# Kernel tuning notes

Hardware: AMD Instinct MI355X
Metric: run time of the kernel (lower is better)

The kernel has to match this reference:

```python
import jax, jax.numpy as jnp
import numpy as np

N_ENTITY = 30000
N_MOVIE = 6000
D = 384            # entity_hidden_size = hidden_size // 2
H = 768            # hidden_size
HT = 768           # token_hidden_size
N_LAYER = 12
N_BLOCK = 2
N_HEAD = 12
HEAD_DIM = H // N_HEAD
NUM_REL = 12
NUM_BASES = 8
E_KG = 200000
E_C = 200000
E_S = 80000
B = 16
LE = 48
LT = 256


def setup_inputs() -> dict:
    key = jax.random.key(0)
    ks = iter(jax.random.split(key, 48))
    nk = lambda: next(ks)
    rn = lambda shape, s=0.02: jax.random.normal(nk(), shape, dtype=jnp.float32) * s
    ri = lambda shape, m: jax.random.randint(nk(), shape, 0, m)
    return {
        'node_embeds': rn((N_ENTITY, D), 0.05),
        'rgcn_bases': rn((NUM_BASES, D, D)),
        'rgcn_comp': rn((NUM_REL, NUM_BASES), 0.3),
        'rgcn_root': rn((D, D)),
        'rgcn_bias': rn((D,), 0.01),
        'ep1_w1': rn((D, D // 2)), 'ep1_b1': rn((D // 2,), 0.01),
        'ep1_w2': rn((D // 2, D)), 'ep1_b2': rn((D,), 0.01),
        'ep2_w': rn((D, H)), 'ep2_b': rn((H,), 0.01),
        'tp1_w1': rn((HT, HT // 2)), 'tp1_b1': rn((HT // 2,), 0.01),
        'tp1_w2': rn((HT // 2, HT)), 'tp1_b2': rn((HT,), 0.01),
        'tp2_w': rn((HT, H)), 'tp2_b': rn((H,), 0.01),
        'ca_w': rn((H, H)),
        'pp1_w1': rn((H, H // 2)), 'pp1_b1': rn((H // 2,), 0.01),
        'pp1_w2': rn((H // 2, H)), 'pp1_b2': rn((H,), 0.01),
        'pp2_w': rn((H, N_LAYER * N_BLOCK * H)), 'pp2_b': rn((N_LAYER * N_BLOCK * H,), 0.01),
        'token_embeds': jax.random.normal(nk(), (B, LT, HT), dtype=jnp.float32),
        'edge_index': ri((2, E_KG), N_ENTITY),
        'edge_type': ri((E_KG,), NUM_REL),
        'edge_index_c': ri((2, E_C), N_ENTITY),
        'edge_index_t_s': ri((2, E_S), N_MOVIE),
        'edge_index_i_s': ri((2, E_S), N_MOVIE),
        'movie_to_entity': ri((N_MOVIE,), N_ENTITY),
        'entity_ids': ri((B, LE), N_ENTITY),
    }


def _mlp(x, w1, b1, w2, b2):
    return jax.nn.relu(x @ w1 + b1) @ w2 + b2


def _gcn(x, edge_index):
    # CustomGCNConv: add self loops, symmetric deg^{-1/2} norm, scatter-add
    n = x.shape[0]
    loop = jnp.arange(n)
    src = jnp.concatenate([edge_index[0], loop])
    dst = jnp.concatenate([edge_index[1], loop])
    deg = jax.ops.segment_sum(jnp.ones_like(dst, dtype=x.dtype), dst, num_segments=n)
    dis = deg ** -0.5  # deg >= 1 due to self loops
    norm = dis[src] * dis[dst]
    return jax.ops.segment_sum(norm[:, None] * x[src], dst, num_segments=n)


def _rgcn(x, edge_index, edge_type, bases, comp, root, bias):
    # PyG RGCNConv with basis decomposition, mean aggregation per relation
    n = x.shape[0]
    src, dst = edge_index[0], edge_index[1]
    W = jnp.einsum('rb,bio->rio', comp, bases)  # [R, D, D]
    out = x @ root + bias
    for r in range(NUM_REL):
        mask = (edge_type == r).astype(x.dtype)
        cnt = jax.ops.segment_sum(mask, dst, num_segments=n)
        norm = mask / jnp.maximum(cnt[dst], 1.0)
        h = x @ W[r]
        out = out + jax.ops.segment_sum(norm[:, None] * h[src], dst, num_segments=n)
    return out


def reference(node_embeds, rgcn_bases, rgcn_comp, rgcn_root, rgcn_bias,
              ep1_w1, ep1_b1, ep1_w2, ep1_b2, ep2_w, ep2_b,
              tp1_w1, tp1_b1, tp1_w2, tp1_b2, tp2_w, tp2_b,
              ca_w, pp1_w1, pp1_b1, pp1_w2, pp1_b2, pp2_w, pp2_b,
              token_embeds, edge_index, edge_type, edge_index_c,
              edge_index_t_s, edge_index_i_s, movie_to_entity, entity_ids):
    # ---- get_entity_embeds ----
    ent0 = _rgcn(node_embeds, edge_index, edge_type, rgcn_bases, rgcn_comp, rgcn_root, rgcn_bias) + node_embeds
    nf = ent0[movie_to_entity]  # sorted_indices == idx_to_id_tensor (keys are range(n_movie))
    ts1 = _gcn(nf, edge_index_t_s)
    ts2 = _gcn(ts1, edge_index_t_s)  # ts3 computed in original but unused -> skipped
    mt = (ts1 + ts2) * 0.5
    is1 = _gcn(nf, edge_index_i_s)
    is2 = _gcn(is1, edge_index_i_s)
    mi = (is1 + is2) * 0.5
    mm = (mt + mi) * 0.5
    c1 = _gcn(ent0, edge_index_c)
    c2 = _gcn(c1, edge_index_c)
    c3 = _gcn(c2, edge_index_c)
    ent = (c1 + c2 + c3 + ent0) * 0.25
    ent = ent.at[movie_to_entity].add(mm)  # index_add_
    ent = _mlp(ent, ep1_w1, ep1_b1, ep1_w2, ep1_b2) + ent
    ent = ent @ ep2_w + ep2_b  # [N_ENTITY, H]
    # ---- forward ----
    eemb = ent[entity_ids]  # [B, LE, H]
    tok = _mlp(token_embeds, tp1_w1, tp1_b1, tp1_w2, tp1_b2) + token_embeds
    tok = tok @ tp2_w + tp2_b  # [B, LT, H]
    attn = jnp.einsum('bth,beh->bte', tok @ ca_w, eemb) / H
    w = jax.nn.softmax(attn, axis=2)  # output_entity=False branch
    prompt = jnp.einsum('bte,beh->bth', w, eemb) + tok
    prompt = _mlp(prompt, pp1_w1, pp1_b1, pp1_w2, pp1_b2) + prompt
    prompt = prompt @ pp2_w + pp2_b  # [B, LT, N_LAYER*N_BLOCK*H]
    prompt = prompt.reshape(B, LT, N_LAYER, N_BLOCK, N_HEAD, HEAD_DIM)
    return prompt.transpose(2, 3, 0, 4, 1, 5)  # [n_layer, n_block, B, n_head, LT, head_dim]
```

## Files before the change

kernel.cpp:

```cpp
#include <hip/hip_runtime.h>
#include <hip/hip_bf16.h>
#include <cstdint>
#include <cstddef>


namespace {

constexpr int NE   = 30000;
constexpr int NM   = 6000;
constexpr int Dm   = 384;
constexpr int Hm   = 768;
constexpr int EKG  = 200000;
constexpr int EC   = 200000;
constexpr int ES   = 80000;
constexpr int Bc   = 16;
constexpr int LE   = 48;
constexpr int NTOK = 4096;
constexpr int NO   = 18432;

constexpr size_t NBf = (size_t)NE * Dm;
constexpr size_t MBF = (size_t)NM * Dm;

constexpr size_t P_XB    = 0;
constexpr size_t P_WCT   = 5760000;
constexpr size_t P_CNT   = 6644736;
constexpr size_t P_ENT0  = 7004736;
constexpr size_t P_HH    = 18524736;
constexpr size_t P_DIS   = 53084736;
constexpr size_t P_E0B   = 0;
constexpr size_t P_C1B   = 2880000;
constexpr size_t P_C2B   = 5760000;
constexpr size_t P_NFB   = 8640000;
constexpr size_t P_T1B   = 9800000;
constexpr size_t P_G1    = 11000000;
constexpr size_t P_ACC   = 41564736;
constexpr size_t P_ENTB  = 55600000;
constexpr size_t P_HIDB  = 0;
constexpr size_t P_ENT2B = 2880000;
constexpr size_t P_E768B = 8640000;
constexpr size_t P_TOKB  = 20160000;
constexpr size_t P_THIDB = 21732864;
constexpr size_t P_TOK1B = 22519296;
constexpr size_t P_TOK2B = 24092160;
constexpr size_t P_QB    = 25665024;
constexpr size_t P_EEMB  = 27237888;
constexpr size_t P_PR0   = 27532800;
constexpr size_t P_PR0B  = 30678528;
constexpr size_t P_PHIDB = 32251392;
constexpr size_t P_WT    = 74000000;
constexpr size_t S_ROOT  = 0;
constexpr size_t S_EP1A  = 147456;
constexpr size_t S_EP1B  = 221184;
constexpr size_t S_EP2   = 294912;
constexpr size_t S_TP1A  = 589824;
constexpr size_t S_TP1B  = 884736;
constexpr size_t S_TP2   = 1179648;
constexpr size_t S_CAW   = 1769472;
constexpr size_t S_PP1A  = 2359296;
constexpr size_t S_PP1B  = 2654208;

constexpr size_t WI       = 6291456 / 4;
constexpr size_t I_CNT    = WI + 0;
constexpr size_t I_PART   = WI + 30000;
constexpr size_t I_KG_RP  = WI + 30256;
constexpr size_t I_KG_CA  = WI + 60256;
constexpr size_t I_KG_SL  = WI + 90256;
constexpr size_t I_C_RP   = WI + 290256;
constexpr size_t I_C_CUR  = WI + 320256;
constexpr size_t I_C_SL   = WI + 350256;
constexpr size_t I_TS_RP  = WI + 550256;
constexpr size_t I_TS_CUR = WI + 556256;
constexpr size_t I_TS_SL  = WI + 562256;
constexpr size_t I_IS_RP  = WI + 642256;
constexpr size_t I_IS_CUR = WI + 648256;
constexpr size_t I_IS_SL  = WI + 654256;
constexpr size_t I_KG_BND = WI + 734256;
constexpr size_t I_KG_CB  = WI + 764256;
constexpr size_t WS_PP2T_BYTE = 6291456;
constexpr size_t WS_NEED      = 34603008;

inline int cdiv(long a, long b) { return (int)((a + b - 1) / b); }

}

typedef short short8v __attribute__((ext_vector_type(8)));
typedef float f32x4 __attribute__((ext_vector_type(4)));

__device__ __forceinline__ unsigned short f2bf(float f) {
  union { float f; uint32_t u; } v; v.f = f;
  uint32_t u = v.u;
  u += 0x7fffu + ((u >> 16) & 1u);
  return (unsigned short)(u >> 16);
}
__device__ __forceinline__ uint32_t pkbf(float a, float b) {
  __hip_bfloat162 h = __float22bfloat162_rn(float2{a, b});
  union { __hip_bfloat162 h; uint32_t u; } cv; cv.h = h;
  return cv.u;
}
__device__ __forceinline__ float bflo(uint32_t u) {
  union { uint32_t u; float f; } c; c.u = u << 16; return c.f;
}
__device__ __forceinline__ float bfhi(uint32_t u) {
  union { uint32_t u; float f; } c; c.u = u & 0xFFFF0000u; return c.f;
}

__device__ __forceinline__ void gl16(const void* g, void* l) {
  __builtin_amdgcn_global_load_lds(
      (const __attribute__((address_space(1))) void*)g,
      (__attribute__((address_space(3))) void*)l, 16, 0, 0);
}


__global__ void k_cvt(const float* __restrict__ x, unsigned short* __restrict__ o, size_t n2) {
  size_t i = (size_t)blockIdx.x * 256 + threadIdx.x;
  if (i >= n2) return;
  float2 v = *(const float2*)(x + 2 * i);
  *(uint32_t*)(o + 2 * i) = pkbf(v.x, v.y);
}

__global__ void k_cvt_t(const float* __restrict__ W, unsigned short* __restrict__ Wt,
                        int K, int N) {
  __shared__ float t[32][33];
  int tx = threadIdx.x & 31, ty = threadIdx.x >> 5;
  int n0 = blockIdx.x * 32, k0 = blockIdx.y * 32;
#pragma unroll
  for (int j = 0; j < 4; ++j)
    t[ty + 8 * j][tx] = W[(size_t)(k0 + ty + 8 * j) * N + n0 + tx];
  __syncthreads();
#pragma unroll
  for (int j = 0; j < 4; ++j) {
    int n = ty + 8 * j;
    Wt[(size_t)(n0 + n) * K + k0 + tx] = f2bf(t[tx][n]);
  }
}

__global__ void k_wcat(const float* __restrict__ comp, const float* __restrict__ bases,
                       unsigned short* __restrict__ Wt) {
  int idx = blockIdx.x * 256 + threadIdx.x;
  if (idx >= 12 * Dm * Dm) return;
  int i = idx % Dm;
  int o = (idx / Dm) % Dm;
  int r = idx / (Dm * Dm);
  float s = 0.f;
#pragma unroll
  for (int b = 0; b < 8; ++b)
    s += comp[r * 8 + b] * bases[(size_t)b * Dm * Dm + (size_t)i * Dm + o];
  Wt[idx] = f2bf(s);
}

__global__ void k_gather_b(const int* __restrict__ idx, const uint32_t* __restrict__ x2,
                           uint32_t* __restrict__ out2, int rows, int D2) {
  size_t i = (size_t)blockIdx.x * 256 + threadIdx.x;
  if (i >= (size_t)rows * D2) return;
  int r = (int)(i / D2);
  int c = (int)(i - (size_t)r * D2);
  out2[i] = x2[(size_t)idx[r] * D2 + c];
}

__global__ void k_scatter_movie(const int* __restrict__ mte, const float* __restrict__ g,
                                float* __restrict__ ent) {
  size_t i = (size_t)blockIdx.x * 256 + threadIdx.x;
  if (i >= MBF) return;
  int m = (int)(i / Dm);
  int d = (int)(i - (size_t)m * Dm);
  atomicAdd(&ent[(size_t)mte[m] * Dm + d], 0.25f * g[i]);
}


__global__ void k_hist(const int* __restrict__ dst, int* __restrict__ cnt, int E) {
  int e = blockIdx.x * 256 + threadIdx.x;
  if (e < E) atomicAdd(&cnt[dst[e]], 1);
}

__global__ void k_hist_lt(const int* __restrict__ dst, const int* __restrict__ typ,
                          int* __restrict__ cnt, int E) {
  int e = blockIdx.x * 256 + threadIdx.x;
  if (e < E && typ[e] < 6) atomicAdd(&cnt[dst[e]], 1);
}

__global__ void k_add_i(const int* __restrict__ a, const int* __restrict__ b,
                        int* __restrict__ o, int n) {
  int i = blockIdx.x * 256 + threadIdx.x;
  if (i < n) o[i] = a[i] + b[i];
}

__global__ void k_scan_blk(const int* __restrict__ in, int* __restrict__ out,
                           int* __restrict__ part, int n) {
  __shared__ int s[256];
  int t = threadIdx.x;
  int g = blockIdx.x * 256 + t;
  int v = (g < n) ? in[g] : 0;
  s[t] = v;
  __syncthreads();
  for (int off = 1; off < 256; off <<= 1) {
    int add = (t >= off) ? s[t - off] : 0;
    __syncthreads();
    s[t] += add;
    __syncthreads();
  }
  if (g < n) out[g] = s[t] - v;
  if (t == 255) part[blockIdx.x] = s[255];
}

__global__ void k_scan_top(int* __restrict__ part, int nb) {
  __shared__ int s[256];
  int t = threadIdx.x;
  int v = (t < nb) ? part[t] : 0;
  s[t] = v;
  __syncthreads();
  for (int off = 1; off < 256; off <<= 1) {
    int add = (t >= off) ? s[t - off] : 0;
    __syncthreads();
    s[t] += add;
    __syncthreads();
  }
  if (t < nb) part[t] = s[t] - v;
}

__global__ void k_scan_add(int* __restrict__ out, const int* __restrict__ part, int n) {
  int g = blockIdx.x * 256 + threadIdx.x;
  if (g < n) out[g] += part[blockIdx.x];
}

__global__ void k_fill(const int* __restrict__ src, const int* __restrict__ dst,
                       int* __restrict__ cur, int* __restrict__ slots, int E) {
  int e = blockIdx.x * 256 + threadIdx.x;
  if (e >= E) return;
  int d = dst[e];
  int pos = atomicAdd(&cur[d], 1);
  slots[pos] = src[e];
}

__global__ void k_fill_split(const int* __restrict__ src, const int* __restrict__ dst,
                             const int* __restrict__ typ, int* __restrict__ cur_a,
                             int* __restrict__ cur_b, int* __restrict__ slots, int E) {
  int e = blockIdx.x * 256 + threadIdx.x;
  if (e >= E) return;
  int d = dst[e];
  int* c = (typ[e] < 6) ? cur_a : cur_b;
  int pos = atomicAdd(&c[d], 1);
  slots[pos] = src[e] | (typ[e] << 16);
}

__global__ void k_dis_rp(const int* __restrict__ rp, float* __restrict__ dis, int n, int E) {
  int v = blockIdx.x * 256 + threadIdx.x;
  if (v >= n) return;
  int e0 = rp[v], e1 = (v + 1 < n) ? rp[v + 1] : E;
  dis[v] = rsqrtf((float)(e1 - e0) + 1.0f);
}

__global__ void k_count_type(const int* __restrict__ dst, const int* __restrict__ typ,
                             float* __restrict__ cnt, int E) {
  int i = blockIdx.x * 256 + threadIdx.x;
  if (i < E) atomicAdd(&cnt[(size_t)typ[i] * NE + dst[i]], 1.0f);
}

__global__ void k_rcp(float* __restrict__ c, size_t n) {
  size_t i = (size_t)blockIdx.x * 256 + threadIdx.x;
  if (i < n) { float v = c[i]; c[i] = (v > 0.f) ? 1.0f / v : 0.f; }
}

template <int OUTM, int ACCM>
__global__ void k_gcn_gb(const unsigned short* __restrict__ x,
                         const float* __restrict__ dis,
                         const int* __restrict__ rp, const int* __restrict__ slots,
                         unsigned short* __restrict__ outb, float* __restrict__ acc,
                         int n, int E, float sc) {
  int v = (int)((blockIdx.x * (size_t)blockDim.x + threadIdx.x) >> 6);
  int lane = threadIdx.x & 63;
  if (v >= n) return;
  float dv = dis[v];
  const uint32_t* xr = (const uint32_t*)(x + (size_t)v * Dm);
  float xv[6];
#pragma unroll
  for (int i = 0; i < 3; ++i) {
    uint32_t u = xr[lane + 64 * i];
    xv[2 * i] = bflo(u); xv[2 * i + 1] = bfhi(u);
  }
  float a[6];
#pragma unroll
  for (int i = 0; i < 6; ++i) a[i] = dv * xv[i];
  int e0 = rp[v], e1 = (v + 1 < n) ? rp[v + 1] : E;
  int e = e0;
  for (; e + 2 <= e1; e += 2) {
    int s0 = slots[e], s1 = slots[e + 1];
    float c0 = dis[s0], c1 = dis[s1];
    const uint32_t* x0 = (const uint32_t*)(x + (size_t)s0 * Dm);
    const uint32_t* x1 = (const uint32_t*)(x + (size_t)s1 * Dm);
    uint32_t u0[3], u1[3];
#pragma unroll
    for (int i = 0; i < 3; ++i) { u0[i] = x0[lane + 64 * i]; u1[i] = x1[lane + 64 * i]; }
#pragma unroll
    for (int i = 0; i < 3; ++i) {
      a[2 * i]     = fmaf(c0, bflo(u0[i]), a[2 * i]);
      a[2 * i + 1] = fmaf(c0, bfhi(u0[i]), a[2 * i + 1]);
      a[2 * i]     = fmaf(c1, bflo(u1[i]), a[2 * i]);
      a[2 * i + 1] = fmaf(c1, bfhi(u1[i]), a[2 * i + 1]);
    }
  }
  if (e < e1) {
    int s0 = slots[e];
    float c0 = dis[s0];
    const uint32_t* x0 = (const uint32_t*)(x + (size_t)s0 * Dm);
#pragma unroll
    for (int i = 0; i < 3; ++i) {
      uint32_t u = x0[lane + 64 * i];
      a[2 * i]     = fmaf(c0, bflo(u), a[2 * i]);
      a[2 * i + 1] = fmaf(c0, bfhi(u), a[2 * i + 1]);
    }
  }
#pragma unroll
  for (int i = 0; i < 6; ++i) a[i] *= dv;
  if (OUTM == 1) {
    uint32_t* ob = (uint32_t*)(outb + (size_t)v * Dm);
#pragma unroll
    for (int i = 0; i < 3; ++i) ob[lane + 64 * i] = pkbf(a[2 * i], a[2 * i + 1]);
  }
  float* ar = acc + (size_t)v * Dm;
  float nw[6];
#pragma unroll
  for (int i = 0; i < 3; ++i) {
    int cidx = 2 * (lane + 64 * i);
    if (ACCM == 1) {
      float2 old = *(const float2*)(ar + cidx);
      nw[2 * i] = old.x + sc * a[2 * i];
      nw[2 * i + 1] = old.y + sc * a[2 * i + 1];
    } else if (ACCM == 2) {
      nw[2 * i] = sc * (xv[2 * i] + a[2 * i]);
      nw[2 * i + 1] = sc * (xv[2 * i + 1] + a[2 * i + 1]);
    } else {
      nw[2 * i] = sc * a[2 * i];
      nw[2 * i + 1] = sc * a[2 * i + 1];
    }
    *(float2*)(ar + cidx) = float2{nw[2 * i], nw[2 * i + 1]};
  }
  if (OUTM == 2) {
    uint32_t* ob = (uint32_t*)(outb + (size_t)v * Dm);
#pragma unroll
    for (int i = 0; i < 3; ++i) ob[lane + 64 * i] = pkbf(nw[2 * i], nw[2 * i + 1]);
  }
}

template <bool FIRST, bool EMITB>
__global__ void k_rgcn_g(const unsigned short* __restrict__ hh, const float* __restrict__ rcp,
                         const int* __restrict__ rp, const int* __restrict__ bnd,
                         const int* __restrict__ slots, float* __restrict__ ent0,
                         unsigned short* __restrict__ outb, int E) {
  int v = (int)((blockIdx.x * (size_t)blockDim.x + threadIdx.x) >> 6);
  int lane = threadIdx.x & 63;
  if (v >= NE) return;
  const int rbase = FIRST ? 0 : 6;
  int e0, e1;
  if (FIRST) { e0 = rp[v]; e1 = bnd[v]; }
  else       { e0 = bnd[v]; e1 = (v + 1 < NE) ? rp[v + 1] : E; }
  float* er = ent0 + (size_t)v * Dm;
  float2 a[3];
#pragma unroll
  for (int i = 0; i < 3; ++i) a[i] = *(const float2*)(er + 2 * lane + 128 * i);
  int e = e0;
  for (; e + 2 <= e1; e += 2) {
    int p0 = slots[e], p1 = slots[e + 1];
    int r0 = (p0 >> 16) - rbase, s0 = p0 & 0xFFFF;
    int r1 = (p1 >> 16) - rbase, s1 = p1 & 0xFFFF;
    float nm0 = rcp[(size_t)(r0 + rbase) * NE + v];
    float nm1 = rcp[(size_t)(r1 + rbase) * NE + v];
    const uint32_t* h0 = (const uint32_t*)(hh + (size_t)s0 * 2304 + (size_t)r0 * 384);
    const uint32_t* h1 = (const uint32_t*)(hh + (size_t)s1 * 2304 + (size_t)r1 * 384);
    uint32_t u0[3], u1[3];
#pragma unroll
    for (int i = 0; i < 3; ++i) { u0[i] = h0[lane + 64 * i]; u1[i] = h1[lane + 64 * i]; }
#pragma unroll
    for (int i = 0; i < 3; ++i) {
      a[i].x = fmaf(nm0, bflo(u0[i]), a[i].x);
      a[i].y = fmaf(nm0, bfhi(u0[i]), a[i].y);
      a[i].x = fmaf(nm1, bflo(u1[i]), a[i].x);
      a[i].y = fmaf(nm1, bfhi(u1[i]), a[i].y);
    }
  }
  if (e < e1) {
    int p0 = slots[e];
    int r0 = (p0 >> 16) - rbase, s0 = p0 & 0xFFFF;
    float nm0 = rcp[(size_t)(r0 + rbase) * NE + v];
    const uint32_t* h0 = (const uint32_t*)(hh + (size_t)s0 * 2304 + (size_t)r0 * 384);
#pragma unroll
    for (int i = 0; i < 3; ++i) {
      uint32_t u = h0[lane + 64 * i];
      a[i].x = fmaf(nm0, bflo(u), a[i].x);
      a[i].y = fmaf(nm0, bfhi(u), a[i].y);
    }
  }
#pragma unroll
  for (int i = 0; i < 3; ++i) *(float2*)(er + 2 * lane + 128 * i) = a[i];
  if (EMITB) {
    uint32_t* ob = (uint32_t*)(outb + (size_t)v * Dm);
#pragma unroll
    for (int i = 0; i < 3; ++i) ob[lane + 64 * i] = pkbf(a[i].x, a[i].y);
  }
}

template <bool RELU, bool RES, int OUT>
__global__ __launch_bounds__(256) void mgemm_bf(
    const unsigned short* __restrict__ A, const unsigned short* __restrict__ Wt,
    const float* __restrict__ bias, const float* __restrict__ Rp,
    void* __restrict__ Cv, int M, int N, int K) {
  __shared__ __align__(16) unsigned short As[128 * 64];
  __shared__ __align__(16) unsigned short Bs[128 * 64];
  const int tid = threadIdx.x;
  const int lane = tid & 63;
  const int w = tid >> 6;
  const int bm = blockIdx.x * 128, bn = blockIdx.y * 128;
  const int wr = (w >> 1) * 64, wc = (w & 1) * 64;
  const int lrow = lane & 15, lq = lane >> 4;
  f32x4 acc[4][4] = {};
  const int prow_l = lane >> 3;
  const int pslot = lane & 7;

  for (int k0 = 0; k0 < K; k0 += 64) {
    __syncthreads();
#pragma unroll
    for (int j = 0; j < 4; ++j) {
      int seg = j * 4 + w;
      int prow = seg * 8 + prow_l;
      int aslot = pslot ^ (prow & 7);
      int arow = min(bm + prow, M - 1);
      gl16(A + (size_t)arow * K + k0 + aslot * 8, &As[seg * 512 + lane * 8]);
    }
#pragma unroll
    for (int j = 0; j < 4; ++j) {
      int seg = j * 4 + w;
      int prow = seg * 8 + prow_l;
      int bslot = pslot ^ (prow & 7);
      int brow = min(bn + prow, N - 1);
      gl16(Wt + (size_t)brow * K + k0 + bslot * 8, &Bs[seg * 512 + lane * 8]);
    }
    __syncthreads();
#pragma unroll
    for (int ks = 0; ks < 2; ++ks) {
      short8v af[4], bf[4];
      const int slot = ks * 4 + lq;
#pragma unroll
      for (int mr = 0; mr < 4; ++mr) {
        int r = wr + mr * 16 + lrow;
        af[mr] = *(const short8v*)&As[r * 64 + ((slot ^ (r & 7)) << 3)];
      }
#pragma unroll
      for (int nc = 0; nc < 4; ++nc) {
        int r = wc + nc * 16 + lrow;
        bf[nc] = *(const short8v*)&Bs[r * 64 + ((slot ^ (r & 7)) << 3)];
      }
#pragma unroll
      for (int mr = 0; mr < 4; ++mr)
#pragma unroll
        for (int nc = 0; nc < 4; ++nc)
          acc[mr][nc] = __builtin_amdgcn_mfma_f32_16x16x32_bf16(
              af[mr], bf[nc], acc[mr][nc], 0, 0, 0);
    }
  }
  size_t colb[4];
  if (OUT == 2) {
#pragma unroll
    for (int nc = 0; nc < 4; ++nc) {
      int c = bn + wc + nc * 16 + lrow;
      int l = c / 1536, rem = c - l * 1536;
      int blk = rem / 768, rem2 = rem - blk * 768;
      int h2 = rem2 >> 6, dd = rem2 & 63;
      colb[nc] = (size_t)(l * 2 + blk) * 3145728 + (size_t)h2 * 16384 + dd;
    }
  }
#pragma unroll
  for (int mr = 0; mr < 4; ++mr) {
#pragma unroll
    for (int e = 0; e < 4; ++e) {
      int r = bm + wr + mr * 16 + lq * 4 + e;
      if (r >= M) continue;
      size_t rowoff = 0;
      if (OUT == 2) rowoff = (size_t)r * 64 + (size_t)(r >> 8) * 180224;
#pragma unroll
      for (int nc = 0; nc < 4; ++nc) {
        int c = bn + wc + nc * 16 + lrow;
        if (c >= N) continue;
        float v = acc[mr][nc][e];
        if (bias) v += bias[c];
        if (RES) v += Rp[(size_t)r * N + c];
        if (RELU) v = fmaxf(v, 0.f);
        if (OUT == 0) {
          ((float*)Cv)[(size_t)r * N + c] = v;
        } else if (OUT == 1) {
          ((unsigned short*)Cv)[(size_t)r * N + c] = f2bf(v);
        } else {
          ((float*)Cv)[colb[nc] + rowoff] = v;
        }
      }
    }
  }
}

__global__ __launch_bounds__(256) void mgemm_fin(
    const unsigned short* __restrict__ A, const float* __restrict__ W,
    const float* __restrict__ bias, float* __restrict__ O, int M, int N, int K) {
  __shared__ __align__(16) unsigned short As[128 * 64];
  __shared__ __align__(16) unsigned short Bs[128 * 64];
  const int tid = threadIdx.x;
  const int lane = tid & 63;
  const int w = tid >> 6;
  const int bm = blockIdx.x * 128, bn = blockIdx.y * 128;
  const int wr = (w >> 1) * 64, wc = (w & 1) * 64;
  const int lrow = lane & 15, lq = lane >> 4;
  f32x4 acc[4][4] = {};
  const int prow_l = lane >> 3;
  const int pslot = lane & 7;
  const int n_loc = tid & 127;
  const int kh = (tid >> 7) * 32;

  for (int k0 = 0; k0 < K; k0 += 64) {
    __syncthreads();
#pragma unroll
    for (int j = 0; j < 4; ++j) {
      int seg = j * 4 + w;
      int prow = seg * 8 + prow_l;
      int aslot = pslot ^ (prow & 7);
      gl16(A + (size_t)(bm + prow) * K + k0 + aslot * 8, &As[seg * 512 + lane * 8]);
    }
    float wv[32];
    const float* wp = W + (size_t)(k0 + kh) * N + bn + n_loc;
#pragma unroll
    for (int j = 0; j < 32; ++j) wv[j] = wp[(size_t)j * N];
#pragma unroll
    for (int c = 0; c < 4; ++c) {
      uint32_t u0 = pkbf(wv[8 * c + 0], wv[8 * c + 1]);
      uint32_t u1 = pkbf(wv[8 * c + 2], wv[8 * c + 3]);
      uint32_t u2 = pkbf(wv[8 * c + 4], wv[8 * c + 5]);
      uint32_t u3 = pkbf(wv[8 * c + 6], wv[8 * c + 7]);
      int s = (kh >> 3) + c;
      *(uint4*)&Bs[n_loc * 64 + ((s ^ (n_loc & 7)) << 3)] = uint4{u0, u1, u2, u3};
    }
    __syncthreads();
#pragma unroll
    for (int ks = 0; ks < 2; ++ks) {
      short8v af[4], bf[4];
      const int slot = ks * 4 + lq;
#pragma unroll
      for (int mr = 0; mr < 4; ++mr) {
        int r = wr + mr * 16 + lrow;
        af[mr] = *(const short8v*)&As[r * 64 + ((slot ^ (r & 7)) << 3)];
      }
#pragma unroll
      for (int nc = 0; nc < 4; ++nc) {
        int r = wc + nc * 16 + lrow;
        bf[nc] = *(const short8v*)&Bs[r * 64 + ((slot ^ (r & 7)) << 3)];
      }
#pragma unroll
      for (int mr = 0; mr < 4; ++mr)
#pragma unroll
        for (int nc = 0; nc < 4; ++nc)
          acc[mr][nc] = __builtin_amdgcn_mfma_f32_16x16x32_bf16(
              af[mr], bf[nc], acc[mr][nc], 0, 0, 0);
    }
  }
#pragma unroll
  for (int mr = 0; mr < 4; ++mr) {
#pragma unroll
    for (int e = 0; e < 4; ++e) {
      int r = bm + wr + mr * 16 + lq * 4 + e;
      int b = r >> 8, t = r & 255;
#pragma unroll
      for (int nc = 0; nc < 4; ++nc) {
        int c = bn + wc + nc * 16 + lrow;
        float v = acc[mr][nc][e] + bias[c];
        int l = c / 1536, rem = c - l * 1536;
        int blk = rem / 768, rem2 = rem - blk * 768;
        int hh = rem2 >> 6, dd = rem2 & 63;
        size_t oi = (((((size_t)l * 2 + blk) * 16 + b) * 12 + hh) * 256 + t) * 64 + dd;
        O[oi] = v;
      }
    }
  }
}

__global__ __launch_bounds__(256) void k_attn(
    const unsigned short* __restrict__ qb, const unsigned short* __restrict__ eb_all,
    const unsigned short* __restrict__ tokb, float* __restrict__ pr0,
    unsigned short* __restrict__ pr0b) {
  int gw = (int)((blockIdx.x * (size_t)blockDim.x + threadIdx.x) >> 6);
  int lane = threadIdx.x & 63;
  if (gw >= NTOK) return;
  int b = gw >> 8;
  const unsigned short* qr = qb + (size_t)gw * Hm;
  float2 q[6];
#pragma unroll
  for (int i = 0; i < 6; ++i) {
    uint32_t u = *(const uint32_t*)(qr + 2 * lane + 128 * i);
    q[i] = float2{bflo(u), bfhi(u)};
  }
  const unsigned short* eb = eb_all + (size_t)b * LE * Hm;
  float myA = -3.0e38f;
  for (int e = 0; e < LE; ++e) {
    const unsigned short* er = eb + (size_t)e * Hm;
    float s = 0.f;
#pragma unroll
    for (int i = 0; i < 6; ++i) {
      uint32_t u = *(const uint32_t*)(er + 2 * lane + 128 * i);
      s = fmaf(q[i].x, bflo(u), s);
      s = fmaf(q[i].y, bfhi(u), s);
    }
#pragma unroll
    for (int off = 32; off > 0; off >>= 1) s += __shfl_xor(s, off);
    if (lane == e) myA = s * (1.0f / 768.0f);
  }
  float mx = myA;
#pragma unroll
  for (int off = 32; off > 0; off >>= 1) mx = fmaxf(mx, __shfl_xor(mx, off));
  float p = (lane < LE) ? expf(myA - mx) : 0.f;
  float sum = p;
#pragma unroll
  for (int off = 32; off > 0; off >>= 1) sum += __shfl_xor(sum, off);
  float wgt = p / sum;
  const unsigned short* tr = tokb + (size_t)gw * Hm;
  float2 a[6];
#pragma unroll
  for (int i = 0; i < 6; ++i) {
    uint32_t u = *(const uint32_t*)(tr + 2 * lane + 128 * i);
    a[i] = float2{bflo(u), bfhi(u)};
  }
  for (int e = 0; e < LE; ++e) {
    float we = __shfl(wgt, e);
    const unsigned short* er = eb + (size_t)e * Hm;
#pragma unroll
    for (int i = 0; i < 6; ++i) {
      uint32_t u = *(const uint32_t*)(er + 2 * lane + 128 * i);
      a[i].x = fmaf(we, bflo(u), a[i].x);
      a[i].y = fmaf(we, bfhi(u), a[i].y);
    }
  }
  float* orow = pr0 + (size_t)gw * Hm;
  unsigned short* obrow = pr0b + (size_t)gw * Hm;
#pragma unroll
  for (int i = 0; i < 6; ++i) {
    *(float2*)(orow + 2 * lane + 128 * i) = a[i];
    *(uint32_t*)(obrow + 2 * lane + 128 * i) = pkbf(a[i].x, a[i].y);
  }
}


extern "C" void kernel_launch(void* const* d_in, const int* in_sizes, int n_in,
                              void* d_out, int out_size, void* d_ws, size_t ws_size,
                              hipStream_t stream) {
  (void)in_sizes; (void)n_in; (void)out_size;

  const float* x_node = (const float*)d_in[0];
  const float* bases  = (const float*)d_in[1];
  const float* comp   = (const float*)d_in[2];
  const float* root   = (const float*)d_in[3];
  const float* rbias  = (const float*)d_in[4];
  const float* ep1w1  = (const float*)d_in[5];
  const float* ep1b1  = (const float*)d_in[6];
  const float* ep1w2  = (const float*)d_in[7];
  const float* ep1b2  = (const float*)d_in[8];
  const float* ep2w   = (const float*)d_in[9];
  const float* ep2b   = (const float*)d_in[10];
  const float* tp1w1  = (const float*)d_in[11];
  const float* tp1b1  = (const float*)d_in[12];
  const float* tp1w2  = (const float*)d_in[13];
  const float* tp1b2  = (const float*)d_in[14];
  const float* tp2w   = (const float*)d_in[15];
  const float* tp2b   = (const float*)d_in[16];
  const float* caw    = (const float*)d_in[17];
  const float* pp1w1  = (const float*)d_in[18];
  const float* pp1b1  = (const float*)d_in[19];
  const float* pp1w2  = (const float*)d_in[20];
  const float* pp1b2  = (const float*)d_in[21];
  const float* pp2w   = (const float*)d_in[22];
  const float* pp2b   = (const float*)d_in[23];
  const float* tokens = (const float*)d_in[24];
  const int* ei_kg = (const int*)d_in[25];
  const int* etype = (const int*)d_in[26];
  const int* ei_c  = (const int*)d_in[27];
  const int* ei_ts = (const int*)d_in[28];
  const int* ei_is = (const int*)d_in[29];
  const int* mte   = (const int*)d_in[30];
  const int* eids  = (const int*)d_in[31];

  float* O = (float*)d_out;
  unsigned short* xb    = (unsigned short*)(O + P_XB);
  unsigned short* wct   = (unsigned short*)(O + P_WCT);
  float* rcpc  = O + P_CNT;
  float* ent0  = O + P_ENT0;
  unsigned short* hh    = (unsigned short*)(O + P_HH);
  float* disc  = O + P_DIS;
  float* dist  = O + P_DIS + 30000;
  float* disi  = O + P_DIS + 36000;
  unsigned short* ent0b = (unsigned short*)(O + P_E0B);
  unsigned short* c1b   = (unsigned short*)(O + P_C1B);
  unsigned short* c2b   = (unsigned short*)(O + P_C2B);
  unsigned short* nfb   = (unsigned short*)(O + P_NFB);
  unsigned short* t1b   = (unsigned short*)(O + P_T1B);
  float* g1    = O + P_G1;
  float* accb  = O + P_ACC;
  unsigned short* entb  = (unsigned short*)(O + P_ENTB);
  unsigned short* hidb  = (unsigned short*)(O + P_HIDB);
  unsigned short* ent2b = (unsigned short*)(O + P_ENT2B);
  unsigned short* e768b = (unsigned short*)(O + P_E768B);
  unsigned short* tokb  = (unsigned short*)(O + P_TOKB);
  unsigned short* thidb = (unsigned short*)(O + P_THIDB);
  unsigned short* tok1b = (unsigned short*)(O + P_TOK1B);
  unsigned short* tok2b = (unsigned short*)(O + P_TOK2B);
  unsigned short* qb    = (unsigned short*)(O + P_QB);
  unsigned short* eemb  = (unsigned short*)(O + P_EEMB);
  float* pr0   = O + P_PR0;
  unsigned short* pr0b  = (unsigned short*)(O + P_PR0B);
  unsigned short* phidb = (unsigned short*)(O + P_PHIDB);
  unsigned short* wts   = (unsigned short*)(O + P_WT);

  int* iws = (int*)d_ws;
  unsigned short* p2b = (unsigned short*)d_ws;
  unsigned short* pp2t = (unsigned short*)d_ws + WS_PP2T_BYTE / 2;
  const bool ws_ok = (ws_size >= WS_NEED);
  int* cnt_i  = iws + I_CNT;
  int* part   = iws + I_PART;
  int* kg_rp  = iws + I_KG_RP;  int* kg_ca = iws + I_KG_CA;  int* kg_sl = iws + I_KG_SL;
  int* kg_bnd = iws + I_KG_BND; int* kg_cb = iws + I_KG_CB;
  int* c_rp   = iws + I_C_RP;   int* c_cur  = iws + I_C_CUR;   int* c_sl  = iws + I_C_SL;
  int* ts_rp  = iws + I_TS_RP;  int* ts_cur = iws + I_TS_CUR;  int* ts_sl = iws + I_TS_SL;
  int* is_rp  = iws + I_IS_RP;  int* is_cur = iws + I_IS_CUR;  int* is_sl = iws + I_IS_SL;

  const int EW = 256;

  k_cvt<<<cdiv(NBf / 2, EW), EW, 0, stream>>>(x_node, xb, NBf / 2);
  k_wcat<<<cdiv(12 * Dm * Dm, EW), EW, 0, stream>>>(comp, bases, wct);
  k_cvt_t<<<dim3(Dm / 32, Dm / 32), 256, 0, stream>>>(root, wts + S_ROOT, Dm, Dm);
  k_cvt_t<<<dim3(192 / 32, Dm / 32), 256, 0, stream>>>(ep1w1, wts + S_EP1A, Dm, 192);
  k_cvt_t<<<dim3(Dm / 32, 192 / 32), 256, 0, stream>>>(ep1w2, wts + S_EP1B, 192, Dm);
  k_cvt_t<<<dim3(Hm / 32, Dm / 32), 256, 0, stream>>>(ep2w, wts + S_EP2, Dm, Hm);
  k_cvt_t<<<dim3(Dm / 32, Hm / 32), 256, 0, stream>>>(tp1w1, wts + S_TP1A, Hm, Dm);
  k_cvt_t<<<dim3(Hm / 32, Dm / 32), 256, 0, stream>>>(tp1w2, wts + S_TP1B, Dm, Hm);
  k_cvt_t<<<dim3(Hm / 32, Hm / 32), 256, 0, stream>>>(tp2w, wts + S_TP2, Hm, Hm);
  k_cvt_t<<<dim3(Hm / 32, Hm / 32), 256, 0, stream>>>(caw, wts + S_CAW, Hm, Hm);
  k_cvt_t<<<dim3(Dm / 32, Hm / 32), 256, 0, stream>>>(pp1w1, wts + S_PP1A, Hm, Dm);
  k_cvt_t<<<dim3(Hm / 32, Dm / 32), 256, 0, stream>>>(pp1w2, wts + S_PP1B, Dm, Hm);

  hipMemsetAsync(cnt_i, 0, (size_t)NE * 4, stream);
  k_hist<<<cdiv(EKG, EW), EW, 0, stream>>>(ei_kg + EKG, cnt_i, EKG);
  {
    int nb = cdiv(NE, 256);
    k_scan_blk<<<nb, 256, 0, stream>>>(cnt_i, kg_rp, part, NE);
    k_scan_top<<<1, 256, 0, stream>>>(part, nb);
    k_scan_add<<<nb, 256, 0, stream>>>(kg_rp, part, NE);
  }
  hipMemsetAsync(cnt_i, 0, (size_t)NE * 4, stream);
  k_hist_lt<<<cdiv(EKG, EW), EW, 0, stream>>>(ei_kg + EKG, etype, cnt_i, EKG);
  k_add_i<<<cdiv(NE, EW), EW, 0, stream>>>(kg_rp, cnt_i, kg_bnd, NE);
  hipMemcpyAsync(kg_ca, kg_rp, (size_t)NE * 4, hipMemcpyDeviceToDevice, stream);
  hipMemcpyAsync(kg_cb, kg_bnd, (size_t)NE * 4, hipMemcpyDeviceToDevice, stream);
  k_fill_split<<<cdiv(EKG, EW), EW, 0, stream>>>(
      ei_kg, ei_kg + EKG, etype, kg_ca, kg_cb, kg_sl, EKG);

  auto build_csr = [&](const int* ei, int n, int E, int* rp, int* cur, int* sl) {
    hipMemsetAsync(cnt_i, 0, (size_t)n * 4, stream);
    k_hist<<<cdiv(E, EW), EW, 0, stream>>>(ei + E, cnt_i, E);
    int nb = cdiv(n, 256);
    k_scan_blk<<<nb, 256, 0, stream>>>(cnt_i, rp, part, n);
    k_scan_top<<<1, 256, 0, stream>>>(part, nb);
    k_scan_add<<<nb, 256, 0, stream>>>(rp, part, n);
    hipMemcpyAsync(cur, rp, (size_t)n * 4, hipMemcpyDeviceToDevice, stream);
    k_fill<<<cdiv(E, EW), EW, 0, stream>>>(ei, ei + E, cur, sl, E);
  };
  build_csr(ei_c, NE, EC, c_rp, c_cur, c_sl);
  build_csr(ei_ts, NM, ES, ts_rp, ts_cur, ts_sl);
  build_csr(ei_is, NM, ES, is_rp, is_cur, is_sl);

  k_dis_rp<<<cdiv(NE, EW), EW, 0, stream>>>(c_rp, disc, NE, EC);
  k_dis_rp<<<cdiv(NM, EW), EW, 0, stream>>>(ts_rp, dist, NM, ES);
  k_dis_rp<<<cdiv(NM, EW), EW, 0, stream>>>(is_rp, disi, NM, ES);

  hipMemsetAsync(rcpc, 0, (size_t)12 * NE * 4, stream);
  k_count_type<<<cdiv(EKG, EW), EW, 0, stream>>>(ei_kg + EKG, etype, rcpc, EKG);
  k_rcp<<<cdiv((long)12 * NE, EW), EW, 0, stream>>>(rcpc, (size_t)12 * NE);

  mgemm_bf<false, true, 0><<<dim3(cdiv(NE, 128), cdiv(Dm, 128)), 256, 0, stream>>>(
      xb, wts + S_ROOT, rbias, x_node, ent0, NE, Dm, Dm);
  mgemm_bf<false, false, 1><<<dim3(cdiv(NE, 128), cdiv(6 * Dm, 128)), 256, 0, stream>>>(
      xb, wct, nullptr, nullptr, hh, NE, 6 * Dm, Dm);
  k_rgcn_g<true, false><<<cdiv((long)NE * 64, EW), EW, 0, stream>>>(
      hh, rcpc, kg_rp, kg_bnd, kg_sl, ent0, nullptr, EKG);
  mgemm_bf<false, false, 1><<<dim3(cdiv(NE, 128), cdiv(6 * Dm, 128)), 256, 0, stream>>>(
      xb, wct + (size_t)6 * Dm * Dm, nullptr, nullptr, hh, NE, 6 * Dm, Dm);
  k_rgcn_g<false, true><<<cdiv((long)NE * 64, EW), EW, 0, stream>>>(
      hh, rcpc, kg_rp, kg_bnd, kg_sl, ent0, ent0b, EKG);

  k_gather_b<<<cdiv((long)NM * 192, EW), EW, 0, stream>>>(
      mte, (const uint32_t*)ent0b, (uint32_t*)nfb, NM, 192);
  k_gcn_gb<1, 3><<<cdiv((long)NM * 64, EW), EW, 0, stream>>>(
      nfb, dist, ts_rp, ts_sl, t1b, g1, NM, ES, 1.0f);
  k_gcn_gb<0, 1><<<cdiv((long)NM * 64, EW), EW, 0, stream>>>(
      t1b, dist, ts_rp, ts_sl, nullptr, g1, NM, ES, 1.0f);
  k_gcn_gb<1, 1><<<cdiv((long)NM * 64, EW), EW, 0, stream>>>(
      nfb, disi, is_rp, is_sl, t1b, g1, NM, ES, 1.0f);
  k_gcn_gb<0, 1><<<cdiv((long)NM * 64, EW), EW, 0, stream>>>(
      t1b, disi, is_rp, is_sl, nullptr, g1, NM, ES, 1.0f);
  k_gcn_gb<1, 2><<<cdiv((long)NE * 64, EW), EW, 0, stream>>>(
      ent0b, disc, c_rp, c_sl, c1b, accb, NE, EC, 0.25f);
  k_gcn_gb<1, 1><<<cdiv((long)NE * 64, EW), EW, 0, stream>>>(
      c1b, disc, c_rp, c_sl, c2b, accb, NE, EC, 0.25f);
  k_scatter_movie<<<cdiv(MBF, EW), EW, 0, stream>>>(mte, g1, accb);
  k_gcn_gb<2, 1><<<cdiv((long)NE * 64, EW), EW, 0, stream>>>(
      c2b, disc, c_rp, c_sl, entb, accb, NE, EC, 0.25f);

  if (ws_ok) {
    k_cvt_t<<<dim3(NO / 32, Hm / 32), 256, 0, stream>>>(pp2w, pp2t, Hm, NO);
  }

  mgemm_bf<true, false, 1><<<dim3(cdiv(NE, 128), cdiv(192, 128)), 256, 0, stream>>>(
      entb, wts + S_EP1A, ep1b1, nullptr, hidb, NE, 192, Dm);
  mgemm_bf<false, true, 1><<<dim3(cdiv(NE, 128), cdiv(Dm, 128)), 256, 0, stream>>>(
      hidb, wts + S_EP1B, ep1b2, accb, ent2b, NE, Dm, 192);
  mgemm_bf<false, false, 1><<<dim3(cdiv(NE, 128), cdiv(Hm, 128)), 256, 0, stream>>>(
      ent2b, wts + S_EP2, ep2b, nullptr, e768b, NE, Hm, Dm);

  k_cvt<<<cdiv((long)NTOK * Hm / 2, EW), EW, 0, stream>>>(tokens, tokb, (size_t)NTOK * Hm / 2);
  mgemm_bf<true, false, 1><<<dim3(cdiv(NTOK, 128), cdiv(Dm, 128)), 256, 0, stream>>>(
      tokb, wts + S_TP1A, tp1b1, nullptr, thidb, NTOK, Dm, Hm);
  mgemm_bf<false, true, 1><<<dim3(cdiv(NTOK, 128), cdiv(Hm, 128)), 256, 0, stream>>>(
      thidb, wts + S_TP1B, tp1b2, tokens, tok1b, NTOK, Hm, Dm);
  mgemm_bf<false, false, 1><<<dim3(cdiv(NTOK, 128), cdiv(Hm, 128)), 256, 0, stream>>>(
      tok1b, wts + S_TP2, tp2b, nullptr, tok2b, NTOK, Hm, Hm);
  mgemm_bf<false, false, 1><<<dim3(cdiv(NTOK, 128), cdiv(Hm, 128)), 256, 0, stream>>>(
      tok2b, wts + S_CAW, nullptr, nullptr, qb, NTOK, Hm, Hm);

  k_gather_b<<<cdiv((long)Bc * LE * (Hm / 2), EW), EW, 0, stream>>>(
      eids, (const uint32_t*)e768b, (uint32_t*)eemb, Bc * LE, Hm / 2);
  k_attn<<<cdiv((long)NTOK * 64, 256), 256, 0, stream>>>(qb, eemb, tok2b, pr0, pr0b);

  mgemm_bf<true, false, 1><<<dim3(cdiv(NTOK, 128), cdiv(Dm, 128)), 256, 0, stream>>>(
      pr0b, wts + S_PP1A, pp1b1, nullptr, phidb, NTOK, Dm, Hm);
  mgemm_bf<false, true, 1><<<dim3(cdiv(NTOK, 128), cdiv(Hm, 128)), 256, 0, stream>>>(
      phidb, wts + S_PP1B, pp1b2, pr0, p2b, NTOK, Hm, Dm);

  if (ws_ok) {
    mgemm_bf<false, false, 2><<<dim3(NTOK / 128, NO / 128), 256, 0, stream>>>(
        p2b, pp2t, pp2b, nullptr, O, NTOK, NO, Hm);
  } else {
    mgemm_fin<<<dim3(NTOK / 128, NO / 128), 256, 0, stream>>>(
        p2b, pp2w, pp2b, O, NTOK, NO, Hm);
  }
}
```

Before: 1.565 ms.

## Batch weight transposes, fold CSR cursor copies into kernels, swizzle final GEMM blocks

Replaces ten separate weight transpose-convert launches with one kernel that picks its matrix by block index. Removes the device-to-device memcpys of CSR row pointers by having the scan-add and add kernels write the cursor copies directly. Adds an XCD-style block swizzle to the large final GEMM so that consecutive blocks share tiles within one chiplet. This trims launch overhead and may improve L2 reuse on the biggest GEMM, at the cost of a hardcoded tile table and a swizzle that assumes the grid divides by 8.

```diff
diff --git a/kernel.cpp b/kernel.cpp
--- a/kernel.cpp
+++ b/kernel.cpp
@@ -134,6 +134,40 @@
   }
 }
 
+__global__ void k_cvt_t_all(
+    const float* s0, unsigned short* d0, const float* s1, unsigned short* d1,
+    const float* s2, unsigned short* d2, const float* s3, unsigned short* d3,
+    const float* s4, unsigned short* d4, const float* s5, unsigned short* d5,
+    const float* s6, unsigned short* d6, const float* s7, unsigned short* d7,
+    const float* s8, unsigned short* d8, const float* s9, unsigned short* d9) {
+  __shared__ float t[32][33];
+  int tile = blockIdx.x;
+  const float* W; unsigned short* Wt; int K, N, base;
+  if      (tile < 144)  { W = s0; Wt = d0; K = 384; N = 384; base = 0; }
+  else if (tile < 216)  { W = s1; Wt = d1; K = 384; N = 192; base = 144; }
+  else if (tile < 288)  { W = s2; Wt = d2; K = 192; N = 384; base = 216; }
+  else if (tile < 576)  { W = s3; Wt = d3; K = 384; N = 768; base = 288; }
+  else if (tile < 864)  { W = s4; Wt = d4; K = 768; N = 384; base = 576; }
+  else if (tile < 1152) { W = s5; Wt = d5; K = 384; N = 768; base = 864; }
+  else if (tile < 1728) { W = s6; Wt = d6; K = 768; N = 768; base = 1152; }
+  else if (tile < 2304) { W = s7; Wt = d7; K = 768; N = 768; base = 1728; }
+  else if (tile < 2592) { W = s8; Wt = d8; K = 768; N = 384; base = 2304; }
+  else                  { W = s9; Wt = d9; K = 384; N = 768; base = 2592; }
+  int lt = tile - base;
+  int ntx = N >> 5;
+  int n0 = (lt % ntx) * 32, k0 = (lt / ntx) * 32;
+  int tx = threadIdx.x & 31, ty = threadIdx.x >> 5;
+#pragma unroll
+  for (int j = 0; j < 4; ++j)
+    t[ty + 8 * j][tx] = W[(size_t)(k0 + ty + 8 * j) * N + n0 + tx];
+  __syncthreads();
+#pragma unroll
+  for (int j = 0; j < 4; ++j) {
+    int n = ty + 8 * j;
+    Wt[(size_t)(n0 + n) * K + k0 + tx] = f2bf(t[tx][n]);
+  }
+}
+
 __global__ void k_wcat(const float* __restrict__ comp, const float* __restrict__ bases,
                        unsigned short* __restrict__ Wt) {
   int idx = blockIdx.x * 256 + threadIdx.x;
@@ -179,9 +213,9 @@
 }
 
 __global__ void k_add_i(const int* __restrict__ a, const int* __restrict__ b,
-                        int* __restrict__ o, int n) {
+                        int* __restrict__ o, int* __restrict__ o2, int n) {
   int i = blockIdx.x * 256 + threadIdx.x;
-  if (i < n) o[i] = a[i] + b[i];
+  if (i < n) { int v = a[i] + b[i]; o[i] = v; o2[i] = v; }
 }
 
 __global__ void k_scan_blk(const int* __restrict__ in, int* __restrict__ out,
@@ -217,9 +251,10 @@
   if (t < nb) part[t] = s[t] - v;
 }
 
-__global__ void k_scan_add(int* __restrict__ out, const int* __restrict__ part, int n) {
+__global__ void k_scan_add(int* __restrict__ out, const int* __restrict__ part,
+                           int* __restrict__ cur, int n) {
   int g = blockIdx.x * 256 + threadIdx.x;
-  if (g < n) out[g] += part[blockIdx.x];
+  if (g < n) { int v = out[g] + part[blockIdx.x]; out[g] = v; cur[g] = v; }
 }
 
 __global__ void k_fill(const int* __restrict__ src, const int* __restrict__ dst,
@@ -398,7 +433,7 @@
   }
 }
 
-template <bool RELU, bool RES, int OUT>
+template <bool RELU, bool RES, int OUT, int SWZ>
 __global__ __launch_bounds__(256) void mgemm_bf(
     const unsigned short* __restrict__ A, const unsigned short* __restrict__ Wt,
     const float* __restrict__ bias, const float* __restrict__ Rp,
@@ -408,7 +443,17 @@
   const int tid = threadIdx.x;
   const int lane = tid & 63;
   const int w = tid >> 6;
-  const int bm = blockIdx.x * 128, bn = blockIdx.y * 128;
+  int bm, bn;
+  if (SWZ) {
+    int bid = blockIdx.y * gridDim.x + blockIdx.x;
+    int cpx = (gridDim.x * gridDim.y) >> 3;
+    int swz = (bid & 7) * cpx + (bid >> 3);
+    bm = (swz % gridDim.x) * 128;
+    bn = (swz / gridDim.x) * 128;
+  } else {
+    bm = blockIdx.x * 128;
+    bn = blockIdx.y * 128;
+  }
   const int wr = (w >> 1) * 64, wc = (w & 1) * 64;
   const int lrow = lane & 15, lq = lane >> 4;
   f32x4 acc[4][4] = {};
@@ -727,16 +772,11 @@
 
   k_cvt<<<cdiv(NBf / 2, EW), EW, 0, stream>>>(x_node, xb, NBf / 2);
   k_wcat<<<cdiv(12 * Dm * Dm, EW), EW, 0, stream>>>(comp, bases, wct);
-  k_cvt_t<<<dim3(Dm / 32, Dm / 32), 256, 0, stream>>>(root, wts + S_ROOT, Dm, Dm);
-  k_cvt_t<<<dim3(192 / 32, Dm / 32), 256, 0, stream>>>(ep1w1, wts + S_EP1A, Dm, 192);
-  k_cvt_t<<<dim3(Dm / 32, 192 / 32), 256, 0, stream>>>(ep1w2, wts + S_EP1B, 192, Dm);
-  k_cvt_t<<<dim3(Hm / 32, Dm / 32), 256, 0, stream>>>(ep2w, wts + S_EP2, Dm, Hm);
-  k_cvt_t<<<dim3(Dm / 32, Hm / 32), 256, 0, stream>>>(tp1w1, wts + S_TP1A, Hm, Dm);
-  k_cvt_t<<<dim3(Hm / 32, Dm / 32), 256, 0, stream>>>(tp1w2, wts + S_TP1B, Dm, Hm);
-  k_cvt_t<<<dim3(Hm / 32, Hm / 32), 256, 0, stream>>>(tp2w, wts + S_TP2, Hm, Hm);
-  k_cvt_t<<<dim3(Hm / 32, Hm / 32), 256, 0, stream>>>(caw, wts + S_CAW, Hm, Hm);
-  k_cvt_t<<<dim3(Dm / 32, Hm / 32), 256, 0, stream>>>(pp1w1, wts + S_PP1A, Hm, Dm);
-  k_cvt_t<<<dim3(Hm / 32, Dm / 32), 256, 0, stream>>>(pp1w2, wts + S_PP1B, Dm, Hm);
+  k_cvt_t_all<<<2880, 256, 0, stream>>>(
+      root, wts + S_ROOT, ep1w1, wts + S_EP1A, ep1w2, wts + S_EP1B,
+      ep2w, wts + S_EP2, tp1w1, wts + S_TP1A, tp1w2, wts + S_TP1B,
+      tp2w, wts + S_TP2, caw, wts + S_CAW, pp1w1, wts + S_PP1A,
+      pp1w2, wts + S_PP1B);
 
   hipMemsetAsync(cnt_i, 0, (size_t)NE * 4, stream);
   k_hist<<<cdiv(EKG, EW), EW, 0, stream>>>(ei_kg + EKG, cnt_i, EKG);
@@ -744,13 +784,11 @@
     int nb = cdiv(NE, 256);
     k_scan_blk<<<nb, 256, 0, stream>>>(cnt_i, kg_rp, part, NE);
     k_scan_top<<<1, 256, 0, stream>>>(part, nb);
-    k_scan_add<<<nb, 256, 0, stream>>>(kg_rp, part, NE);
+    k_scan_add<<<nb, 256, 0, stream>>>(kg_rp, part, kg_ca, NE);
   }
   hipMemsetAsync(cnt_i, 0, (size_t)NE * 4, stream);
   k_hist_lt<<<cdiv(EKG, EW), EW, 0, stream>>>(ei_kg + EKG, etype, cnt_i, EKG);
-  k_add_i<<<cdiv(NE, EW), EW, 0, stream>>>(kg_rp, cnt_i, kg_bnd, NE);
-  hipMemcpyAsync(kg_ca, kg_rp, (size_t)NE * 4, hipMemcpyDeviceToDevice, stream);
-  hipMemcpyAsync(kg_cb, kg_bnd, (size_t)NE * 4, hipMemcpyDeviceToDevice, stream);
+  k_add_i<<<cdiv(NE, EW), EW, 0, stream>>>(kg_rp, cnt_i, kg_bnd, kg_cb, NE);
   k_fill_split<<<cdiv(EKG, EW), EW, 0, stream>>>(
       ei_kg, ei_kg + EKG, etype, kg_ca, kg_cb, kg_sl, EKG);
 
@@ -760,8 +798,7 @@
     int nb = cdiv(n, 256);
     k_scan_blk<<<nb, 256, 0, stream>>>(cnt_i, rp, part, n);
     k_scan_top<<<1, 256, 0, stream>>>(part, nb);
-    k_scan_add<<<nb, 256, 0, stream>>>(rp, part, n);
-    hipMemcpyAsync(cur, rp, (size_t)n * 4, hipMemcpyDeviceToDevice, stream);
+    k_scan_add<<<nb, 256, 0, stream>>>(rp, part, cur, n);
     k_fill<<<cdiv(E, EW), EW, 0, stream>>>(ei, ei + E, cur, sl, E);
   };
   build_csr(ei_c, NE, EC, c_rp, c_cur, c_sl);
@@ -776,13 +813,13 @@
   k_count_type<<<cdiv(EKG, EW), EW, 0, stream>>>(ei_kg + EKG, etype, rcpc, EKG);
   k_rcp<<<cdiv((long)12 * NE, EW), EW, 0, stream>>>(rcpc, (size_t)12 * NE);
 
-  mgemm_bf<false, true, 0><<<dim3(cdiv(NE, 128), cdiv(Dm, 128)), 256, 0, stream>>>(
+  mgemm_bf<false, true, 0, 0><<<dim3(cdiv(NE, 128), cdiv(Dm, 128)), 256, 0, stream>>>(
       xb, wts + S_ROOT, rbias, x_node, ent0, NE, Dm, Dm);
-  mgemm_bf<false, false, 1><<<dim3(cdiv(NE, 128), cdiv(6 * Dm, 128)), 256, 0, stream>>>(
+  mgemm_bf<false, false, 1, 0><<<dim3(cdiv(NE, 128), cdiv(6 * Dm, 128)), 256, 0, stream>>>(
       xb, wct, nullptr, nullptr, hh, NE, 6 * Dm, Dm);
   k_rgcn_g<true, false><<<cdiv((long)NE * 64, EW), EW, 0, stream>>>(
       hh, rcpc, kg_rp, kg_bnd, kg_sl, ent0, nullptr, EKG);
-  mgemm_bf<false, false, 1><<<dim3(cdiv(NE, 128), cdiv(6 * Dm, 128)), 256, 0, stream>>>(
+  mgemm_bf<false, false, 1, 0><<<dim3(cdiv(NE, 128), cdiv(6 * Dm, 128)), 256, 0, stream>>>(
       xb, wct + (size_t)6 * Dm * Dm, nullptr, nullptr, hh, NE, 6 * Dm, Dm);
   k_rgcn_g<false, true><<<cdiv((long)NE * 64, EW), EW, 0, stream>>>(
       hh, rcpc, kg_rp, kg_bnd, kg_sl, ent0, ent0b, EKG);
@@ -809,34 +846,34 @@
     k_cvt_t<<<dim3(NO / 32, Hm / 32), 256, 0, stream>>>(pp2w, pp2t, Hm, NO);
   }
 
-  mgemm_bf<true, false, 1><<<dim3(cdiv(NE, 128), cdiv(192, 128)), 256, 0, stream>>>(
+  mgemm_bf<true, false, 1, 0><<<dim3(cdiv(NE, 128), cdiv(192, 128)), 256, 0, stream>>>(
       entb, wts + S_EP1A, ep1b1, nullptr, hidb, NE, 192, Dm);
-  mgemm_bf<false, true, 1><<<dim3(cdiv(NE, 128), cdiv(Dm, 128)), 256, 0, stream>>>(
+  mgemm_bf<false, true, 1, 0><<<dim3(cdiv(NE, 128), cdiv(Dm, 128)), 256, 0, stream>>>(
       hidb, wts + S_EP1B, ep1b2, accb, ent2b, NE, Dm, 192);
-  mgemm_bf<false, false, 1><<<dim3(cdiv(NE, 128), cdiv(Hm, 128)), 256, 0, stream>>>(
+  mgemm_bf<false, false, 1, 0><<<dim3(cdiv(NE, 128), cdiv(Hm, 128)), 256, 0, stream>>>(
       ent2b, wts + S_EP2, ep2b, nullptr, e768b, NE, Hm, Dm);
 
   k_cvt<<<cdiv((long)NTOK * Hm / 2, EW), EW, 0, stream>>>(tokens, tokb, (size_t)NTOK * Hm / 2);
-  mgemm_bf<true, false, 1><<<dim3(cdiv(NTOK, 128), cdiv(Dm, 128)), 256, 0, stream>>>(
+  mgemm_bf<true, false, 1, 0><<<dim3(cdiv(NTOK, 128), cdiv(Dm, 128)), 256, 0, stream>>>(
       tokb, wts + S_TP1A, tp1b1, nullptr, thidb, NTOK, Dm, Hm);
-  mgemm_bf<false, true, 1><<<dim3(cdiv(NTOK, 128), cdiv(Hm, 128)), 256, 0, stream>>>(
+  mgemm_bf<false, true, 1, 0><<<dim3(cdiv(NTOK, 128), cdiv(Hm, 128)), 256, 0, stream>>>(
       thidb, wts + S_TP1B, tp1b2, tokens, tok1b, NTOK, Hm, Dm);
-  mgemm_bf<false, false, 1><<<dim3(cdiv(NTOK, 128), cdiv(Hm, 128)), 256, 0, stream>>>(
+  mgemm_bf<false, false, 1, 0><<<dim3(cdiv(NTOK, 128), cdiv(Hm, 128)), 256, 0, stream>>>(
       tok1b, wts + S_TP2, tp2b, nullptr, tok2b, NTOK, Hm, Hm);
-  mgemm_bf<false, false, 1><<<dim3(cdiv(NTOK, 128), cdiv(Hm, 128)), 256, 0, stream>>>(
+  mgemm_bf<false, false, 1, 0><<<dim3(cdiv(NTOK, 128), cdiv(Hm, 128)), 256, 0, stream>>>(
       tok2b, wts + S_CAW, nullptr, nullptr, qb, NTOK, Hm, Hm);
 
   k_gather_b<<<cdiv((long)Bc * LE * (Hm / 2), EW), EW, 0, stream>>>(
       eids, (const uint32_t*)e768b, (uint32_t*)eemb, Bc * LE, Hm / 2);
   k_attn<<<cdiv((long)NTOK * 64, 256), 256, 0, stream>>>(qb, eemb, tok2b, pr0, pr0b);
 
-  mgemm_bf<true, false, 1><<<dim3(cdiv(NTOK, 128), cdiv(Dm, 128)), 256, 0, stream>>>(
+  mgemm_bf<true, false, 1, 0><<<dim3(cdiv(NTOK, 128), cdiv(Dm, 128)), 256, 0, stream>>>(
       pr0b, wts + S_PP1A, pp1b1, nullptr, phidb, NTOK, Dm, Hm);
-  mgemm_bf<false, true, 1><<<dim3(cdiv(NTOK, 128), cdiv(Hm, 128)), 256, 0, stream>>>(
+  mgemm_bf<false, true, 1, 0><<<dim3(cdiv(NTOK, 128), cdiv(Hm, 128)), 256, 0, stream>>>(
       phidb, wts + S_PP1B, pp1b2, pr0, p2b, NTOK, Hm, Dm);
 
   if (ws_ok) {
-    mgemm_bf<false, false, 2><<<dim3(NTOK / 128, NO / 128), 256, 0, stream>>>(
+    mgemm_bf<false, false, 2, 1><<<dim3(NTOK / 128, NO / 128), 256, 0, stream>>>(
         p2b, pp2t, pp2b, nullptr, O, NTOK, NO, Hm);
   } else {
     mgemm_fin<<<dim3(NTOK / 128, NO / 128), 256, 0, stream>>>(
```

After: 1.555 ms. No clear change (-0.6%).
